# Optimization experiments

Measured on AMD Instinct MI355X. Metric: run time of the kernel, lower is better.

The kernel has to match this reference:

```python
import jax, jax.numpy as jnp
import numpy as np

ALPHA = 0.2   # LeakyReLU negative slope (init arg alpha)
H = 256       # hidden_dim
U = 1024      # user pairs -> 2U user nodes
M = 64        # UAV nodes
D = 2 * U     # uniform out-degree per UAV (edges sorted by source)
N = 2 * U + M
E = M * D


def _lstm_dir(x, w_ih, w_hh, b):
    # x: [T, B, I] -> outputs [T, B, Hc]; b = b_ih + b_hh (they only ever add)
    Hc = w_hh.shape[1]
    B = x.shape[1]
    def step(carry, xt):
        h, c = carry
        g = xt @ w_ih.T + h @ w_hh.T + b          # [B, 4*Hc], gate order i,f,g,o
        i, f, gg, o = jnp.split(g, 4, axis=-1)
        c = jax.nn.sigmoid(f) * c + jax.nn.sigmoid(i) * jnp.tanh(gg)
        h = jax.nn.sigmoid(o) * jnp.tanh(c)
        return (h, c), h
    h0 = jnp.zeros((B, Hc), x.dtype)
    _, hs = jax.lax.scan(step, (h0, h0), x)
    return hs


def _bilstm(x, wih, whh, b):
    # wih: [2, 4Hc, I]; whh: [2, 4Hc, Hc]; b: [2, 4Hc]; dir 0 = fwd, 1 = reverse
    fwd = _lstm_dir(x, wih[0], whh[0], b[0])
    rev = _lstm_dir(x[::-1], wih[1], whh[1], b[1])[::-1]
    return jnp.concatenate([fwd, rev], axis=-1)   # [T, B, 2*Hc]


def _mlp2(h, w1, b1, w2, b2):
    h = jax.nn.relu(h @ w1.T + b1)
    return jax.nn.relu(h @ w2.T + b2)


def _forward(x, edge_index, users_num,
             ul_wih, ul_whh, ul_b, uav_lin_w, uav_lin_b,
             msg_w1, msg_b1, msg_w2, msg_b2,
             wq_w, wq_b, wr_w, wr_b, att_w, att_b,
             upd_w1, upd_b1, upd_w2, upd_b2,
             uavl_wih, uavl_whh, uavl_b, lin2_w, lin2_b):
    Un = users_num
    n = x.shape[0]
    m = n - 2 * Un
    # ---- users bidirectional LSTM over the pair (seq_len=2, batch=U) ----
    seq = jnp.stack([x[:Un], x[Un:2 * Un]], axis=0)        # [2, U, 2]
    users = _bilstm(seq, ul_wih, ul_whh, ul_b)             # [2, U, H]
    users = jnp.concatenate([users[0], users[1]], axis=0)  # [2U, H]
    uavs = x[2 * Un:] @ uav_lin_w.T + uav_lin_b            # [M, H]
    h = jnp.concatenate([users, uavs], axis=0)             # [N, H]
    # ---- message passing (flow target_to_source: i=src, aggregate at src) ----
    src, tgt = edge_index[0], edge_index[1]
    xi = h[src]                                            # [E, H]
    xj = h[tgt]                                            # [E, H]
    msg = _mlp2(jnp.concatenate([xi, xj], axis=1), msg_w1, msg_b1, msg_w2, msg_b2)  # [E, H]
    q = xi @ wq_w.T + wq_b
    r = msg @ wr_w.T + wr_b
    a = jax.nn.leaky_relu(jnp.concatenate([q, r], axis=1) @ att_w.T + att_b, ALPHA)  # [E,1]
    # segment softmax: edges sorted by source, uniform degree -> reshape [M, D]
    a = jax.nn.softmax(a.reshape(m, -1), axis=1).reshape(-1, 1)
    # ---- scatter-mean aggregate over source index ----
    agg = jax.ops.segment_sum(a * msg, src, num_segments=n)          # [N, H]
    cnt = jax.ops.segment_sum(jnp.ones((src.shape[0],), x.dtype), src, num_segments=n)
    agg = agg / jnp.maximum(cnt, 1.0)[:, None]
    # ---- update ----
    h2 = _mlp2(jnp.concatenate([agg, h], axis=1), upd_w1, upd_b1, upd_w2, upd_b2)  # [N, H]
    uav_seq = h2[2 * Un:][:, None, :]                      # [M, 1, H]
    uav_out = _bilstm(uav_seq, uavl_wih, uavl_whh, uavl_b)[:, 0, :]  # [M, H]
    out = jnp.concatenate([h2[:2 * Un], uav_out], axis=0)
    return jax.nn.sigmoid(out @ lin2_w.T + lin2_b)         # [N, 2]


def setup_inputs():
    key = jax.random.key(0)
    ks = iter(jax.random.split(key, 32))
    p = lambda *s: jax.random.normal(next(ks), s, jnp.float32) * 0.05
    Hc = H // 2
    x = jax.random.uniform(next(ks), (N, 2), jnp.float32)
    src = jnp.repeat(2 * U + jnp.arange(M), D)
    tgt = jnp.tile(jnp.arange(2 * U), M)
    edge_index = jnp.stack([src, tgt]).astype(jnp.int32)
    return dict(
        x=x, edge_index=edge_index, users_num=U,
        ul_wih=p(2, 4 * Hc, 2), ul_whh=p(2, 4 * Hc, Hc), ul_b=p(2, 4 * Hc),
        uav_lin_w=p(H, 2), uav_lin_b=p(H),
        msg_w1=p(H, 2 * H), msg_b1=p(H), msg_w2=p(H, H), msg_b2=p(H),
        wq_w=p(H, H), wq_b=p(H), wr_w=p(H, H), wr_b=p(H),
        att_w=p(1, 2 * H), att_b=p(1),
        upd_w1=p(H, 2 * H), upd_b1=p(H), upd_w2=p(H, H), upd_b2=p(H),
        uavl_wih=p(2, 4 * Hc, H), uavl_whh=p(2, 4 * Hc, Hc), uavl_b=p(2, 4 * Hc),
        lin2_w=p(2, H), lin2_b=p(2),
    )


def reference(x, edge_index, users_num,
              ul_wih, ul_whh, ul_b, uav_lin_w, uav_lin_b,
              msg_w1, msg_b1, msg_w2, msg_b2,
              wq_w, wq_b, wr_w, wr_b, att_w, att_b,
              upd_w1, upd_b1, upd_w2, upd_b2,
              uavl_wih, uavl_whh, uavl_b, lin2_w, lin2_b):
    return _forward(x, edge_index, users_num,
                    ul_wih, ul_whh, ul_b, uav_lin_w, uav_lin_b,
                    msg_w1, msg_b1, msg_w2, msg_b2,
                    wq_w, wq_b, wr_w, wr_b, att_w, att_b,
                    upd_w1, upd_b1, upd_w2, upd_b2,
                    uavl_wih, uavl_whh, uavl_b, lin2_w, lin2_b)
```

## Files before the change

### kernel.cpp

```cpp
#include <hip/hip_runtime.h>
#include <hip/hip_bf16.h>
#include <math.h>

#define UQ   1024
#define NUQ  2048
#define MQ   64
#define NN   2112
#define HD   256

typedef __attribute__((ext_vector_type(4))) float f32x4;
typedef __attribute__((ext_vector_type(2))) float f32x2;
typedef __attribute__((ext_vector_type(8))) __bf16 bf16x8;

#define OFF_HB    0u
#define OFF_HUF   65536u
#define OFF_PUBF  1146880u
#define OFF_PB    2195456u
#define OFF_SPR   2260992u
#define OFF_ATT   2261248u
#define OFF_WHHT  2263552u
#define OFF_WIHT  2787840u
#define OFF_W1F   3836416u
#define OFF_W2F   4098560u
#define OFF_UW1F  4229632u
#define OFF_UW2F  4491776u
#define OFF_CREC  4622848u
#define OFF_H2U   5155328u
#define OFF_PART  5220864u

__device__ __forceinline__ float sigm(float v) { return 1.f / (1.f + expf(-v)); }

__device__ __forceinline__ int huf_idx(int row, int k) {
  return (((row >> 6) * 8 + (k >> 5)) * 4 + ((row >> 4) & 3)) * 512 +
         (((k >> 3) & 3) * 16 + (row & 15)) * 8 + (k & 7);
}

__device__ __forceinline__ void gl16(const void* g, void* l) {
  __builtin_amdgcn_global_load_lds((const __attribute__((address_space(1))) void*)g,
                                   (__attribute__((address_space(3))) void*)l, 16, 0, 0);
}

__device__ __forceinline__ int2 pack_fp8x8(const float v[8]) {
  int lo = 0, hi = 0;
  lo = __builtin_amdgcn_cvt_pk_fp8_f32(v[0], v[1], lo, false);
  lo = __builtin_amdgcn_cvt_pk_fp8_f32(v[2], v[3], lo, true);
  hi = __builtin_amdgcn_cvt_pk_fp8_f32(v[4], v[5], hi, false);
  hi = __builtin_amdgcn_cvt_pk_fp8_f32(v[6], v[7], hi, true);
  return make_int2(lo, hi);
}

__device__ void tile_transpose_perm(const float* __restrict__ in, int in_ld,
                                    float* __restrict__ out, int out_ld,
                                    int k0, int c0) {
  __shared__ float ldt[64][68];
  const int t = threadIdx.x;
  {
    const int ci = t >> 2, kq = t & 3;
    const int c = c0 + ci;
    const int row = (c & 3) * 128 + (c >> 2);
    const float* src = in + row * in_ld + k0 + kq * 16;
#pragma unroll
    for (int e = 0; e < 4; ++e)
      *(f32x4*)&ldt[ci][kq * 16 + e * 4] = *(const f32x4*)(src + e * 4);
  }
  __syncthreads();
  {
    const int kk = t >> 2, cq = t & 3;
    float* dst = out + (k0 + kk) * out_ld + c0 + cq * 16;
#pragma unroll
    for (int e4 = 0; e4 < 4; ++e4) {
      f32x4 v;
#pragma unroll
      for (int j = 0; j < 4; ++j) v[j] = ldt[cq * 16 + e4 * 4 + j][kk];
      *(f32x4*)(dst + e4 * 4) = v;
    }
  }
}

template<int K>
__device__ void frag_cast16(const float* __restrict__ W, int j0, __bf16* __restrict__ frag) {
  __shared__ float ldc[16][K + 4];
  const int t = threadIdx.x;
  {
    const int jr = t >> 4, kq = t & 15;
    const float* src = W + (j0 + jr) * K + kq * (K / 16);
#pragma unroll
    for (int e = 0; e < K / 64; ++e)
      *(f32x4*)&ldc[jr][kq * (K / 16) + e * 4] = *(const f32x4*)(src + e * 4);
  }
  __syncthreads();
  const int f = j0 >> 4;
  constexpr int nks = K >> 5;
  constexpr int thr_per_ks = 256 / nks;
  constexpr int q_per_thr = 512 / thr_per_ks;
  const int ks = t / thr_per_ks;
  const int q0 = (t % thr_per_ks) * q_per_thr;
#pragma unroll
  for (int h = 0; h < q_per_thr / 8; ++h) {
    bf16x8 v;
#pragma unroll
    for (int e = 0; e < 8; ++e) {
      int q = q0 + h * 8 + e;
      int lane = q >> 3;
      v[e] = (__bf16)ldc[lane & 15][ks * 32 + (lane >> 4) * 8 + (q & 7)];
    }
    *(bf16x8*)(frag + (ks * 16 + f) * 512 + q0 + h * 8) = v;
  }
}

__device__ void frag_cast16_fp8(const float* __restrict__ W, int j0, char* __restrict__ frag) {
  __shared__ float ldc[16][260];
  const int t = threadIdx.x;
  {
    const int jr = t >> 4, kq = t & 15;
    const float* src = W + (j0 + jr) * 256 + kq * 16;
#pragma unroll
    for (int e = 0; e < 4; ++e)
      *(f32x4*)&ldc[jr][kq * 16 + e * 4] = *(const f32x4*)(src + e * 4);
  }
  __syncthreads();
  const int f = j0 >> 4;
  const int ks = t >> 5;
  const int q0 = (t & 31) * 16;
#pragma unroll
  for (int h = 0; h < 2; ++h) {
    const int qb = q0 + h * 8;
    const int lane = qb >> 3;
    float v[8];
#pragma unroll
    for (int e = 0; e < 8; ++e)
      v[e] = ldc[lane & 15][ks * 32 + (lane >> 4) * 8 + e];
    *(int2*)(frag + (ks * 16 + f) * 512 + qb) = pack_fp8x8(v);
  }
}

__global__ __launch_bounds__(256) void k0_prep(
    const float* __restrict__ ul_whh, const float* __restrict__ uavl_wih,
    const float* __restrict__ msg_w1, const float* __restrict__ msg_w2,
    const float* __restrict__ upd_w1, const float* __restrict__ upd_w2,
    const float* __restrict__ att_w,  const float* __restrict__ att_b,
    const float* __restrict__ wq_w,   const float* __restrict__ wq_b,
    const float* __restrict__ wr_w,   const float* __restrict__ wr_b,
    char* __restrict__ ws)
{
  const int b = blockIdx.x, t = threadIdx.x;
  if (b < 32) {
    const int dir = b >> 4, tile = b & 15;
    tile_transpose_perm(ul_whh + dir * 65536, 128,
                        (float*)(ws + OFF_WHHT) + dir * 65536, 512,
                        (tile >> 3) * 64, (tile & 7) * 64);
  } else if (b < 96) {
    const int b2 = b - 32, dir = b2 >> 5, tile = b2 & 31;
    tile_transpose_perm(uavl_wih + dir * 131072, 256,
                        (float*)(ws + OFF_WIHT) + dir * 131072, 512,
                        (tile >> 3) * 64, (tile & 7) * 64);
  } else if (b < 112) {
    frag_cast16_fp8(msg_w2, (b - 96) * 16, (char*)(ws + OFF_W2F));
  } else if (b < 128) {
    frag_cast16<512>(msg_w1, (b - 112) * 16, (__bf16*)(ws + OFF_W1F));
  } else if (b < 144) {
    frag_cast16<512>(upd_w1, (b - 128) * 16, (__bf16*)(ws + OFF_UW1F));
  } else if (b < 160) {
    frag_cast16<256>(upd_w2, (b - 144) * 16, (__bf16*)(ws + OFF_UW2F));
  } else {
    float* wqa = (float*)(ws + OFF_ATT);
    float* vv  = wqa + 256;
    float* c0  = wqa + 512;
    float sa = 0.f, sr = 0.f;
    for (int j = 0; j < 256; ++j) {
      sa += att_w[j]       * wq_w[j * 256 + t];
      sr += att_w[256 + j] * wr_w[j * 256 + t];
    }
    wqa[t] = sa; vv[t] = sr;
    __shared__ float red[256];
    red[t] = att_w[t] * wq_b[t] + att_w[256 + t] * wr_b[t];
    __syncthreads();
    for (int s = 128; s > 0; s >>= 1) { if (t < s) red[t] += red[t + s]; __syncthreads(); }
    if (t == 0) c0[0] = red[0] + att_b[0];
  }
}

__global__ __launch_bounds__(256) void k1_embed(
    const float* __restrict__ x, const float* __restrict__ ul_wih,
    const float* __restrict__ ul_b, const float* __restrict__ uav_lin_w,
    const float* __restrict__ uav_lin_b, char* __restrict__ ws)
{
  __bf16* huf = (__bf16*)(ws + OFF_HUF);
  const int b = blockIdx.x, tid = threadIdx.x;
  if (b < 256) {
    const float* whhT = (const float*)(ws + OFF_WHHT);
    const int dir = tid >> 7, hc = tid & 127;
    const int u0 = b * 4;
    float wx[4], wy[4], bb[4];
#pragma unroll
    for (int g = 0; g < 4; ++g) {
      int row = g * 128 + hc;
      wx[g] = ul_wih[dir * 1024 + row * 2 + 0];
      wy[g] = ul_wih[dir * 1024 + row * 2 + 1];
      bb[g] = ul_b[dir * 512 + row];
    }
    __shared__ float h1s[2][128][4];
    __shared__ float hout[8][260];
    float c1[4], h1v[4], in1x[4], in1y[4];
#pragma unroll
    for (int uu = 0; uu < 4; ++uu) {
      int u = u0 + uu;
      float ax = x[u * 2], ay = x[u * 2 + 1];
      float bx = x[(UQ + u) * 2], by = x[(UQ + u) * 2 + 1];
      float i0x = dir ? bx : ax, i0y = dir ? by : ay;
      in1x[uu] = dir ? ax : bx; in1y[uu] = dir ? ay : by;
      float gv[4];
#pragma unroll
      for (int g = 0; g < 4; ++g) gv[g] = wx[g] * i0x + wy[g] * i0y + bb[g];
      float ii = sigm(gv[0]), gg = tanhf(gv[2]), oo = sigm(gv[3]);
      c1[uu] = ii * gg;
      h1v[uu] = oo * tanhf(c1[uu]);
      h1s[dir][hc][uu] = h1v[uu];
    }
    __syncthreads();
    float acc[4][4];
#pragma unroll
    for (int uu = 0; uu < 4; ++uu)
#pragma unroll
      for (int g = 0; g < 4; ++g) acc[uu][g] = wx[g] * in1x[uu] + wy[g] * in1y[uu] + bb[g];
#pragma unroll 4
    for (int k = 0; k < 128; ++k) {
      f32x4 hv  = *(const f32x4*)&h1s[dir][k][0];
      f32x4 wv4 = *(const f32x4*)(whhT + dir * 65536 + k * 512 + hc * 4);
#pragma unroll
      for (int uu = 0; uu < 4; ++uu)
#pragma unroll
        for (int g = 0; g < 4; ++g) acc[uu][g] += hv[uu] * wv4[g];
    }
    const int col = dir * 128 + hc;
#pragma unroll
    for (int uu = 0; uu < 4; ++uu) {
      float ii = sigm(acc[uu][0]), ff = sigm(acc[uu][1]);
      float gg = tanhf(acc[uu][2]), oo = sigm(acc[uu][3]);
      float c2 = ff * c1[uu] + ii * gg;
      float h2v = oo * tanhf(c2);
      float va = dir ? h2v : h1v[uu];
      float vb = dir ? h1v[uu] : h2v;
      hout[uu][col] = va;
      hout[4 + uu][col] = vb;
    }
    __syncthreads();
    {
      const int lr = tid >> 5, c = tid & 31;
      bf16x8 v;
#pragma unroll
      for (int e = 0; e < 8; ++e) v[e] = (__bf16)hout[lr][c * 8 + e];
      const int node = (lr < 4) ? (u0 + lr) : (UQ + u0 + lr - 4);
      *(bf16x8*)(huf + huf_idx(node, c * 8)) = v;
    }
  } else {
    float* hb = (float*)(ws + OFF_HB);
    const int j = tid;
    const int mb = (b - 256) * 16;
    for (int m = mb; m < mb + 16; ++m) {
      float xa = x[(NUQ + m) * 2], xb = x[(NUQ + m) * 2 + 1];
      float val = xa * uav_lin_w[j * 2] + xb * uav_lin_w[j * 2 + 1] + uav_lin_b[j];
      hb[m * 256 + j] = val;
      huf[huf_idx(NUQ + m, j)] = (__bf16)val;
    }
  }
}

template<int G, int NKS>
__device__ __forceinline__ void frag_gemm_acc_g(const __bf16* __restrict__ Abase, int g0,
                                                const __bf16* __restrict__ Bbase,
                                                f32x4 acc[G][4]) {
  const int lane = threadIdx.x & 63;
  const int cg = (threadIdx.x >> 6) & 3;
  for (int ks = 0; ks < NKS; ++ks) {
    bf16x8 Af[G], Bf[4];
#pragma unroll
    for (int g = 0; g < G; ++g)
      Af[g] = *(const bf16x8*)(Abase + ((ks * 4 + g0 + g) * 64 + lane) * 8);
#pragma unroll
    for (int f = 0; f < 4; ++f)
      Bf[f] = *(const bf16x8*)(Bbase + ((ks * 16 + cg * 4 + f) * 64 + lane) * 8);
#pragma unroll
    for (int g = 0; g < G; ++g)
#pragma unroll
      for (int f = 0; f < 4; ++f)
        acc[g][f] = __builtin_amdgcn_mfma_f32_16x16x32_bf16(Af[g], Bf[f], acc[g][f], 0, 0, 0);
  }
}

__global__ __launch_bounds__(256) void k2_proj(const float* __restrict__ msg_b1,
                                               char* __restrict__ ws)
{
  const __bf16* huf = (const __bf16*)(ws + OFF_HUF);
  const __bf16* w1f = (const __bf16*)(ws + OFF_W1F);
  const int b = blockIdx.x;
  const int tid = threadIdx.x;
  const int lane = tid & 63, cg = tid >> 6;
  const int cl = lane & 15, g16 = lane >> 4;
  if (b < 64) {
    f32x4 acc[2][4] = {};
    frag_gemm_acc_g<2, 8>(huf + (b >> 1) * 16384, (b & 1) * 2, w1f + 65536, acc);
    __shared__ float ldt[32][264];
#pragma unroll
    for (int g = 0; g < 2; ++g)
#pragma unroll
      for (int f = 0; f < 4; ++f)
#pragma unroll
        for (int r = 0; r < 4; ++r)
          ldt[g * 16 + g16 * 4 + r][cg * 64 + f * 16 + cl] = acc[g][f][r];
    __syncthreads();
    char* pubf = (char*)(ws + OFF_PUBF);
    const int c2 = b >> 3, r16base = (b & 7) * 2;
#pragma unroll
    for (int p = 0; p < 4; ++p) {
      const int region = p * 4 + (tid >> 6);
      const int ks = region >> 1, r16l = region & 1;
      const int row15 = tid & 15, kg = (tid >> 4) & 3;
      const int row = r16l * 16 + row15;
      float v[8];
#pragma unroll
      for (int j = 0; j < 8; ++j) v[j] = ldt[row][ks * 32 + kg * 8 + j];
      const int dst = ((c2 * 8 + ks) * 16 + (r16base + r16l)) * 512 + (kg * 16 + row15) * 8;
      *(int2*)(pubf + dst) = pack_fp8x8(v);
    }
  } else if (b == 64) {
    f32x4 acc[4][4] = {};
    frag_gemm_acc_g<4, 8>(huf + 32 * 16384, 0, w1f, acc);
    float* pb = (float*)(ws + OFF_PB);
#pragma unroll
    for (int g = 0; g < 4; ++g)
#pragma unroll
      for (int f = 0; f < 4; ++f)
#pragma unroll
        for (int r = 0; r < 4; ++r) {
          int row = g * 16 + g16 * 4 + r;
          int col = cg * 64 + f * 16 + cl;
          pb[row * 256 + col] = acc[g][f][r] + msg_b1[col];
        }
  } else {
    const float* hb  = (const float*)(ws + OFF_HB);
    const float* wqa = (const float*)(ws + OFF_ATT);
    const float* c0  = wqa + 512;
    float* spr = (float*)(ws + OFF_SPR);
    if (tid < 64) {
      float s = 0.f;
      for (int k = 0; k < 256; ++k) s += hb[tid * 256 + k] * wqa[k];
      spr[tid] = s + c0[0];
    }
  }
}

__global__ __launch_bounds__(1024, 2) void k3_edge(const float* __restrict__ msg_b2,
                                                   char* __restrict__ ws)
{
  const char*  PUBF = (const char*)(ws + OFF_PUBF);
  const float* PB   = (const float*)(ws + OFF_PB);
  const float* spr  = (const float*)(ws + OFF_SPR);
  const float* vv   = (const float*)(ws + OFF_ATT) + 256;
  const char*  W2F  = (const char*)(ws + OFF_W2F);
  float* crec = (float*)(ws + OFF_CREC);

  __shared__ __align__(16) char bufA[2][8192];
  __shared__ __align__(16) char bufB[2][8192];
  __shared__ float plds[16][64];
  __shared__ float redmax[16], wds[16];
  __shared__ float wvs[4][256];

  const int m = blockIdx.x >> 3, ch = blockIdx.x & 7;
  const int tid = threadIdx.x, wave = tid >> 6, lane = tid & 63;
  const int cl = lane & 15, g16 = lane >> 4;
  const int rg = wave >> 2, cg = wave & 3;
  const int rot = (m + ch) & 7;
  const float sm = spr[m];
  const char* Asrc = PUBF + ch * 65536;
  const float* pbm = PB + m * 256;
  const int bq = ((tid >> 4) & 3) * 8;

  auto repack = [](int2 raw, f32x4 p0, f32x4 p1) -> int2 {
    f32x2 a01 = __builtin_amdgcn_cvt_pk_f32_fp8(raw.x, false);
    f32x2 a23 = __builtin_amdgcn_cvt_pk_f32_fp8(raw.x, true);
    f32x2 a45 = __builtin_amdgcn_cvt_pk_f32_fp8(raw.y, false);
    f32x2 a67 = __builtin_amdgcn_cvt_pk_f32_fp8(raw.y, true);
    float v[8];
    v[0] = fmaxf(a01.x + p0[0], 0.f);
    v[1] = fmaxf(a01.y + p0[1], 0.f);
    v[2] = fmaxf(a23.x + p0[2], 0.f);
    v[3] = fmaxf(a23.y + p0[3], 0.f);
    v[4] = fmaxf(a45.x + p1[0], 0.f);
    v[5] = fmaxf(a45.y + p1[1], 0.f);
    v[6] = fmaxf(a67.x + p1[2], 0.f);
    v[7] = fmaxf(a67.y + p1[3], 0.f);
    return pack_fp8x8(v);
  };

  {
    int2 raw = *(const int2*)(Asrc + rot * 8192 + tid * 8);
    if (wave < 8)
      gl16(W2F + rot * 8192 + wave * 1024 + lane * 16, &bufB[0][wave * 1024 + lane * 16]);
    const float* pbp = pbm + rot * 32 + bq;
    f32x4 p0 = *(const f32x4*)pbp, p1 = *(const f32x4*)(pbp + 4);
    *(int2*)(&bufA[0][tid * 8]) = repack(raw, p0, p1);
  }
  __syncthreads();

  f32x4 acc[4][4] = {};
  for (int i = 0; i < 8; ++i) {
    const int cur = i & 1;
    int2 arn = make_int2(0, 0);
    f32x4 pn0{}, pn1{};
    if (i < 7) {
      const int ksn = (i + 1 + rot) & 7;
      arn = *(const int2*)(Asrc + ksn * 8192 + tid * 8);
      if (wave < 8)
        gl16(W2F + ksn * 8192 + wave * 1024 + lane * 16, &bufB[cur ^ 1][wave * 1024 + lane * 16]);
      const float* pbp = pbm + ksn * 32 + bq;
      pn0 = *(const f32x4*)pbp;
      pn1 = *(const f32x4*)(pbp + 4);
    }
    long Af[4], Bf[4];
#pragma unroll
    for (int g = 0; g < 4; ++g)
      Af[g] = *(const long*)(&bufA[cur][((rg * 4 + g) * 64 + lane) * 8]);
#pragma unroll
    for (int f = 0; f < 4; ++f)
      Bf[f] = *(const long*)(&bufB[cur][((cg * 4 + f) * 64 + lane) * 8]);
    __builtin_amdgcn_s_setprio(1);
#pragma unroll
    for (int g = 0; g < 4; ++g)
#pragma unroll
      for (int f = 0; f < 4; ++f)
        acc[g][f] = __builtin_amdgcn_mfma_f32_16x16x32_fp8_fp8(Af[g], Bf[f], acc[g][f], 0, 0, 0);
    __builtin_amdgcn_s_setprio(0);
    if (i < 7) {
      *(int2*)(&bufA[cur ^ 1][tid * 8]) = repack(arn, pn0, pn1);
    }
    __syncthreads();
  }

  float p[4][4] = {};
#pragma unroll
  for (int f = 0; f < 4; ++f) {
    const int j = cg * 64 + f * 16 + cl;
    const float b2j = msg_b2[j], vj = vv[j];
#pragma unroll
    for (int g = 0; g < 4; ++g)
#pragma unroll
      for (int r = 0; r < 4; ++r) {
        float mv = fmaxf(acc[g][f][r] + b2j, 0.f);
        acc[g][f][r] = mv;
        p[g][r] += mv * vj;
      }
  }
#pragma unroll
  for (int mask = 1; mask < 16; mask <<= 1)
#pragma unroll
    for (int g = 0; g < 4; ++g)
#pragma unroll
      for (int r = 0; r < 4; ++r) p[g][r] += __shfl_xor(p[g][r], mask);
  if (cl == 0) {
#pragma unroll
    for (int g = 0; g < 4; ++g)
#pragma unroll
      for (int r = 0; r < 4; ++r) plds[wave][g * 16 + g16 * 4 + r] = p[g][r];
  }
  __syncthreads();

  float lr[4][4], wm = -3.4e38f;
#pragma unroll
  for (int g = 0; g < 4; ++g)
#pragma unroll
    for (int r = 0; r < 4; ++r) {
      int row = g * 16 + g16 * 4 + r;
      float l = plds[rg * 4 + 0][row] + plds[rg * 4 + 1][row] +
                plds[rg * 4 + 2][row] + plds[rg * 4 + 3][row] + sm;
      l = l > 0.f ? l : 0.2f * l;
      lr[g][r] = l;
      wm = fmaxf(wm, l);
    }
  wm = fmaxf(wm, __shfl_xor(wm, 16));
  wm = fmaxf(wm, __shfl_xor(wm, 32));
  if (lane == 0) redmax[wave] = wm;
  __syncthreads();
  float Mc = redmax[0];
#pragma unroll
  for (int i = 1; i < 16; ++i) Mc = fmaxf(Mc, redmax[i]);

  float e[4][4], ds = 0.f;
#pragma unroll
  for (int g = 0; g < 4; ++g)
#pragma unroll
    for (int r = 0; r < 4; ++r) { e[g][r] = __expf(lr[g][r] - Mc); ds += e[g][r]; }
  ds += __shfl_xor(ds, 16);
  ds += __shfl_xor(ds, 32);
  if (lane == 0) wds[wave] = ds;

#pragma unroll
  for (int f = 0; f < 4; ++f) {
    float w = 0.f;
#pragma unroll
    for (int g = 0; g < 4; ++g)
#pragma unroll
      for (int r = 0; r < 4; ++r) w += e[g][r] * acc[g][f][r];
    w += __shfl_xor(w, 16);
    w += __shfl_xor(w, 32);
    if (g16 == 0) wvs[rg][cg * 64 + f * 16 + cl] = w;
  }
  __syncthreads();

  float* rec = crec + (m * 8 + ch) * 260;
  if (tid < 256) rec[tid] = wvs[0][tid] + wvs[1][tid] + wvs[2][tid] + wvs[3][tid];
  if (tid == 0) rec[256] = Mc;
  if (tid == 1) rec[257] = wds[0] + wds[4] + wds[8] + wds[12];
}

__global__ __launch_bounds__(256) void k56_update(
    const float* __restrict__ upd_b1, const float* __restrict__ upd_b2,
    const float* __restrict__ lin2_w, const float* __restrict__ lin2_b,
    float* __restrict__ out, char* __restrict__ ws)
{
  const __bf16* huf  = (const __bf16*)(ws + OFF_HUF);
  const __bf16* uw1f = (const __bf16*)(ws + OFF_UW1F);
  const __bf16* uw2f = (const __bf16*)(ws + OFF_UW2F);

  __shared__ __align__(16) __bf16 l1f[8 * 2 * 512];
  __shared__ __align__(16) __bf16 aggf[8 * 2 * 512];
  __shared__ float scs[32][8];
  __shared__ float sS[32];
  __shared__ float l2p[4][32][2];

  const int b = blockIdx.x, tid = threadIdx.x;
  const int lane = tid & 63, cg = tid >> 6;
  const int cl = lane & 15, g16 = lane >> 4;

  f32x4 acc[2][4] = {};
  if (b < 64) {
    frag_gemm_acc_g<2, 8>(huf + (b >> 1) * 16384, (b & 1) * 2, uw1f + 8 * 16 * 512, acc);
  } else {
    const int m0 = (b - 64) * 32;
    const float* crec = (const float*)(ws + OFF_CREC);
    if (tid < 32) {
      const int m = m0 + tid;
      float mx = -3.4e38f;
      for (int c = 0; c < 8; ++c) mx = fmaxf(mx, crec[(m * 8 + c) * 260 + 256]);
      float S = 0.f;
      for (int c = 0; c < 8; ++c) {
        float sc = __expf(crec[(m * 8 + c) * 260 + 256] - mx);
        scs[tid][c] = sc;
        S += sc * crec[(m * 8 + c) * 260 + 257];
      }
      sS[tid] = S;
    }
    __syncthreads();
    for (int ml = 0; ml < 32; ++ml) {
      float A = 0.f;
#pragma unroll
      for (int c = 0; c < 8; ++c) A += scs[ml][c] * crec[((m0 + ml) * 8 + c) * 260 + tid];
      float agg = A / sS[ml] * (1.f / 2048.f);
      aggf[((tid >> 5) * 2 + (ml >> 4)) * 512 + (((tid >> 3) & 3) * 16 + (ml & 15)) * 8 + (tid & 7)] =
          (__bf16)agg;
    }
    __syncthreads();
    const int g0 = (b - 64) * 2;
    const __bf16* hufu = huf + 32 * 16384;
    for (int ks = 0; ks < 8; ++ks) {
      bf16x8 Af[2], Bf[4];
#pragma unroll
      for (int g = 0; g < 2; ++g)
        Af[g] = *(const bf16x8*)(aggf + ((ks * 2 + g) * 64 + lane) * 8);
#pragma unroll
      for (int f = 0; f < 4; ++f)
        Bf[f] = *(const bf16x8*)(uw1f + ((ks * 16 + cg * 4 + f) * 64 + lane) * 8);
#pragma unroll
      for (int g = 0; g < 2; ++g)
#pragma unroll
        for (int f = 0; f < 4; ++f)
          acc[g][f] = __builtin_amdgcn_mfma_f32_16x16x32_bf16(Af[g], Bf[f], acc[g][f], 0, 0, 0);
    }
    for (int ks = 8; ks < 16; ++ks) {
      bf16x8 Af[2], Bf[4];
#pragma unroll
      for (int g = 0; g < 2; ++g)
        Af[g] = *(const bf16x8*)(hufu + (((ks - 8) * 4 + g0 + g) * 64 + lane) * 8);
#pragma unroll
      for (int f = 0; f < 4; ++f)
        Bf[f] = *(const bf16x8*)(uw1f + ((ks * 16 + cg * 4 + f) * 64 + lane) * 8);
#pragma unroll
      for (int g = 0; g < 2; ++g)
#pragma unroll
        for (int f = 0; f < 4; ++f)
          acc[g][f] = __builtin_amdgcn_mfma_f32_16x16x32_bf16(Af[g], Bf[f], acc[g][f], 0, 0, 0);
    }
  }

#pragma unroll
  for (int g = 0; g < 2; ++g)
#pragma unroll
    for (int f = 0; f < 4; ++f) {
      const int col = cg * 64 + f * 16 + cl;
      const float b1 = upd_b1[col];
#pragma unroll
      for (int r = 0; r < 4; ++r) {
        float v = fmaxf(acc[g][f][r] + b1, 0.f);
        l1f[((col >> 5) * 2 + g) * 512 + (((col >> 3) & 3) * 16 + g16 * 4 + r) * 8 + (col & 7)] =
            (__bf16)v;
      }
    }
  __syncthreads();

  f32x4 a2[2][4] = {};
  for (int ks = 0; ks < 8; ++ks) {
    bf16x8 Af[2], Bf[4];
#pragma unroll
    for (int g = 0; g < 2; ++g)
      Af[g] = *(const bf16x8*)(l1f + ((ks * 2 + g) * 64 + lane) * 8);
#pragma unroll
    for (int f = 0; f < 4; ++f)
      Bf[f] = *(const bf16x8*)(uw2f + ((ks * 16 + cg * 4 + f) * 64 + lane) * 8);
#pragma unroll
    for (int g = 0; g < 2; ++g)
#pragma unroll
      for (int f = 0; f < 4; ++f)
        a2[g][f] = __builtin_amdgcn_mfma_f32_16x16x32_bf16(Af[g], Bf[f], a2[g][f], 0, 0, 0);
  }

  if (b < 64) {
    float d0[2][4] = {}, d1[2][4] = {};
#pragma unroll
    for (int f = 0; f < 4; ++f) {
      const int col = cg * 64 + f * 16 + cl;
      const float b2 = upd_b2[col];
      const float w0 = lin2_w[col], w1 = lin2_w[256 + col];
#pragma unroll
      for (int g = 0; g < 2; ++g)
#pragma unroll
        for (int r = 0; r < 4; ++r) {
          float hv = fmaxf(a2[g][f][r] + b2, 0.f);
          d0[g][r] += hv * w0;
          d1[g][r] += hv * w1;
        }
    }
#pragma unroll
    for (int mask = 1; mask < 16; mask <<= 1)
#pragma unroll
      for (int g = 0; g < 2; ++g)
#pragma unroll
        for (int r = 0; r < 4; ++r) {
          d0[g][r] += __shfl_xor(d0[g][r], mask);
          d1[g][r] += __shfl_xor(d1[g][r], mask);
        }
    if (cl == 0) {
#pragma unroll
      for (int g = 0; g < 2; ++g)
#pragma unroll
        for (int r = 0; r < 4; ++r) {
          l2p[cg][g * 16 + g16 * 4 + r][0] = d0[g][r];
          l2p[cg][g * 16 + g16 * 4 + r][1] = d1[g][r];
        }
    }
    __syncthreads();
    if (tid < 32) {
      float s0 = l2p[0][tid][0] + l2p[1][tid][0] + l2p[2][tid][0] + l2p[3][tid][0] + lin2_b[0];
      float s1 = l2p[0][tid][1] + l2p[1][tid][1] + l2p[2][tid][1] + l2p[3][tid][1] + lin2_b[1];
      const int row = b * 32 + tid;
      out[row * 2 + 0] = 1.f / (1.f + expf(-s0));
      out[row * 2 + 1] = 1.f / (1.f + expf(-s1));
    }
  } else {
    float* h2u = (float*)(ws + OFF_H2U);
    const int m0 = (b - 64) * 32;
#pragma unroll
    for (int g = 0; g < 2; ++g)
#pragma unroll
      for (int f = 0; f < 4; ++f) {
        const int col = cg * 64 + f * 16 + cl;
        const float b2 = upd_b2[col];
#pragma unroll
        for (int r = 0; r < 4; ++r) {
          const int rl = g * 16 + g16 * 4 + r;
          h2u[(m0 + rl) * 256 + col] = fmaxf(a2[g][f][r] + b2, 0.f);
        }
      }
  }
}

__global__ __launch_bounds__(256) void k7a_gates(char* __restrict__ ws)
{
  const float* h2u  = (const float*)(ws + OFF_H2U);
  const float* wihT = (const float*)(ws + OFF_WIHT);
  float* part = (float*)(ws + OFF_PART);
  const int m = blockIdx.x >> 2, kq = blockIdx.x & 3;
  const int tid = threadIdx.x;
  const int dir = tid >> 7, hc = tid & 127;
  __shared__ float xs[64];
  if (tid < 64) xs[tid] = h2u[m * 256 + kq * 64 + tid];
  __syncthreads();
  f32x4 a4 = {0.f, 0.f, 0.f, 0.f};
  for (int k = 0; k < 64; ++k) {
    float xv = xs[k];
    f32x4 wv4 = *(const f32x4*)(wihT + dir * 131072 + (kq * 64 + k) * 512 + hc * 4);
#pragma unroll
    for (int g = 0; g < 4; ++g) a4[g] += xv * wv4[g];
  }
  *(f32x4*)(part + (m * 4 + kq) * 1024 + dir * 512 + hc * 4) = a4;
}

__global__ __launch_bounds__(256) void k7b_final(
    const float* __restrict__ uavl_b, const float* __restrict__ lin2_w,
    const float* __restrict__ lin2_b, float* __restrict__ out, char* __restrict__ ws)
{
  const float* part = (const float*)(ws + OFF_PART);
  const int m = blockIdx.x, tid = threadIdx.x;
  const int dir = tid >> 7, hc = tid & 127;
  f32x4 a4 = {0.f, 0.f, 0.f, 0.f};
#pragma unroll
  for (int kq = 0; kq < 4; ++kq) {
    f32x4 p = *(const f32x4*)(part + (m * 4 + kq) * 1024 + dir * 512 + hc * 4);
#pragma unroll
    for (int g = 0; g < 4; ++g) a4[g] += p[g];
  }
  float bb[4];
#pragma unroll
  for (int g = 0; g < 4; ++g) bb[g] = uavl_b[dir * 512 + g * 128 + hc];
  __shared__ float uo[256];
  float ii = sigm(a4[0] + bb[0]);
  float gg = tanhf(a4[2] + bb[2]);
  float oo = sigm(a4[3] + bb[3]);
  float cc = ii * gg;
  uo[dir * 128 + hc] = oo * tanhf(cc);
  __syncthreads();
  float p0 = uo[tid] * lin2_w[tid];
  float p1 = uo[tid] * lin2_w[256 + tid];
#pragma unroll
  for (int mask = 1; mask < 64; mask <<= 1) {
    p0 += __shfl_xor(p0, mask);
    p1 += __shfl_xor(p1, mask);
  }
  __shared__ float r0s[4], r1s[4];
  const int lane = tid & 63, wv = tid >> 6;
  if (lane == 0) { r0s[wv] = p0; r1s[wv] = p1; }
  __syncthreads();
  if (tid == 0) {
    float d0 = r0s[0] + r0s[1] + r0s[2] + r0s[3] + lin2_b[0];
    float d1 = r1s[0] + r1s[1] + r1s[2] + r1s[3] + lin2_b[1];
    out[(NUQ + m) * 2 + 0] = 1.f / (1.f + expf(-d0));
    out[(NUQ + m) * 2 + 1] = 1.f / (1.f + expf(-d1));
  }
}

extern "C" void kernel_launch(void* const* d_in, const int* in_sizes, int n_in,
                              void* d_out, int out_size, void* d_ws, size_t ws_size,
                              hipStream_t stream)
{
  const float* x         = (const float*)d_in[0];
  const float* ul_wih    = (const float*)d_in[3];
  const float* ul_whh    = (const float*)d_in[4];
  const float* ul_b      = (const float*)d_in[5];
  const float* uav_lin_w = (const float*)d_in[6];
  const float* uav_lin_b = (const float*)d_in[7];
  const float* msg_w1    = (const float*)d_in[8];
  const float* msg_b1    = (const float*)d_in[9];
  const float* msg_w2    = (const float*)d_in[10];
  const float* msg_b2    = (const float*)d_in[11];
  const float* wq_w      = (const float*)d_in[12];
  const float* wq_b      = (const float*)d_in[13];
  const float* wr_w      = (const float*)d_in[14];
  const float* wr_b      = (const float*)d_in[15];
  const float* att_w     = (const float*)d_in[16];
  const float* att_b     = (const float*)d_in[17];
  const float* upd_w1    = (const float*)d_in[18];
  const float* upd_b1    = (const float*)d_in[19];
  const float* upd_w2    = (const float*)d_in[20];
  const float* upd_b2    = (const float*)d_in[21];
  const float* uavl_wih  = (const float*)d_in[22];
  const float* uavl_b    = (const float*)d_in[24];
  const float* lin2_w    = (const float*)d_in[25];
  const float* lin2_b    = (const float*)d_in[26];
  char* ws = (char*)d_ws;
  float* out = (float*)d_out;

  k0_prep<<<dim3(161), dim3(256), 0, stream>>>(ul_whh, uavl_wih, msg_w1, msg_w2, upd_w1,
                                               upd_w2, att_w, att_b, wq_w, wq_b, wr_w, wr_b, ws);
  k1_embed<<<dim3(260), dim3(256), 0, stream>>>(x, ul_wih, ul_b, uav_lin_w, uav_lin_b, ws);
  k2_proj<<<dim3(66), dim3(256), 0, stream>>>(msg_b1, ws);
  k3_edge<<<dim3(512), dim3(1024), 0, stream>>>(msg_b2, ws);
  k56_update<<<dim3(66), dim3(256), 0, stream>>>(upd_b1, upd_b2, lin2_w, lin2_b, out, ws);
  k7a_gates<<<dim3(256), dim3(256), 0, stream>>>(ws);
  k7b_final<<<dim3(64), dim3(256), 0, stream>>>(uavl_b, lin2_w, lin2_b, out, ws);
}
```

Measured before the change: 92.54 us.

## Fuse update, UAV LSTM gates and final linear into one kernel with fp16 MFMA

```diff
diff --git a/kernel.cpp b/kernel.cpp
--- a/kernel.cpp
+++ b/kernel.cpp
@@ -1,5 +1,6 @@
 #include <hip/hip_runtime.h>
 #include <hip/hip_bf16.h>
+#include <hip/hip_fp16.h>
 #include <math.h>
 
 #define UQ   1024
@@ -11,22 +12,22 @@
 typedef __attribute__((ext_vector_type(4))) float f32x4;
 typedef __attribute__((ext_vector_type(2))) float f32x2;
 typedef __attribute__((ext_vector_type(8))) __bf16 bf16x8;
+typedef __attribute__((ext_vector_type(8))) _Float16 f16x8;
 
 #define OFF_HB    0u
 #define OFF_HUF   65536u
 #define OFF_PUBF  1146880u
-#define OFF_PB    2195456u
-#define OFF_SPR   2260992u
-#define OFF_ATT   2261248u
-#define OFF_WHHT  2263552u
-#define OFF_WIHT  2787840u
-#define OFF_W1F   3836416u
-#define OFF_W2F   4098560u
-#define OFF_UW1F  4229632u
-#define OFF_UW2F  4491776u
-#define OFF_CREC  4622848u
-#define OFF_H2U   5155328u
-#define OFF_PART  5220864u
+#define OFF_PB    1671168u
+#define OFF_SPR   1736704u
+#define OFF_ATT   1736960u
+#define OFF_WHHT  1739264u
+#define OFF_W1F   2263552u
+#define OFF_W2F   2525696u
+#define OFF_UW1F  2591232u
+#define OFF_UW2F  2853376u
+#define OFF_CREC  2984448u
+#define OFF_WIHF  3516928u
+#define OFF_H2UF  4041216u
 
 __device__ __forceinline__ float sigm(float v) { return 1.f / (1.f + expf(-v)); }
 
@@ -149,19 +150,38 @@
     tile_transpose_perm(ul_whh + dir * 65536, 128,
                         (float*)(ws + OFF_WHHT) + dir * 65536, 512,
                         (tile >> 3) * 64, (tile & 7) * 64);
+  } else if (b < 48) {
+    frag_cast16_fp8(msg_w2, (b - 32) * 16, (char*)(ws + OFF_W2F));
+  } else if (b < 64) {
+    frag_cast16<512>(msg_w1, (b - 48) * 16, (__bf16*)(ws + OFF_W1F));
+  } else if (b < 80) {
+    frag_cast16<512>(upd_w1, (b - 64) * 16, (__bf16*)(ws + OFF_UW1F));
   } else if (b < 96) {
-    const int b2 = b - 32, dir = b2 >> 5, tile = b2 & 31;
-    tile_transpose_perm(uavl_wih + dir * 131072, 256,
-                        (float*)(ws + OFF_WIHT) + dir * 131072, 512,
-                        (tile >> 3) * 64, (tile & 7) * 64);
-  } else if (b < 112) {
-    frag_cast16_fp8(msg_w2, (b - 96) * 16, (char*)(ws + OFF_W2F));
-  } else if (b < 128) {
-    frag_cast16<512>(msg_w1, (b - 112) * 16, (__bf16*)(ws + OFF_W1F));
-  } else if (b < 144) {
-    frag_cast16<512>(upd_w1, (b - 128) * 16, (__bf16*)(ws + OFF_UW1F));
+    frag_cast16<256>(upd_w2, (b - 80) * 16, (__bf16*)(ws + OFF_UW2F));
   } else if (b < 160) {
-    frag_cast16<256>(upd_w2, (b - 144) * 16, (__bf16*)(ws + OFF_UW2F));
+    __shared__ float ldc2[16][260];
+    const int b2 = b - 96;
+    {
+      const int jr = t >> 4, kq = t & 15;
+      const int jp = b2 * 16 + jr;
+      const int dir = jp >> 9, rem = jp & 511, hc = rem >> 2, gg = rem & 3;
+      const float* src = uavl_wih + (dir * 512 + gg * 128 + hc) * 256 + kq * 16;
+#pragma unroll
+      for (int e = 0; e < 4; ++e)
+        *(f32x4*)&ldc2[jr][kq * 16 + e * 4] = *(const f32x4*)(src + e * 4);
+    }
+    __syncthreads();
+    _Float16* wf = (_Float16*)(ws + OFF_WIHF);
+    const int ks = t >> 5, sub = t & 31;
+#pragma unroll
+    for (int i = 0; i < 2; ++i) {
+      const int gp = sub * 2 + i;
+      const int cl = gp & 15, g16 = gp >> 4;
+      _Float16 v[8];
+#pragma unroll
+      for (int e = 0; e < 8; ++e) v[e] = (_Float16)ldc2[cl][ks * 32 + g16 * 8 + e];
+      *(ulong2*)(wf + (ks * 64 + b2) * 512 + (g16 * 16 + cl) * 8) = *(ulong2*)v;
+    }
   } else {
     float* wqa = (float*)(ws + OFF_ATT);
     float* vv  = wqa + 256;
@@ -513,117 +533,56 @@
   if (tid == 1) rec[257] = wds[0] + wds[4] + wds[8] + wds[12];
 }
 
-__global__ __launch_bounds__(256) void k56_update(
+__global__ __launch_bounds__(1024) void k567_update(
     const float* __restrict__ upd_b1, const float* __restrict__ upd_b2,
-    const float* __restrict__ lin2_w, const float* __restrict__ lin2_b,
-    float* __restrict__ out, char* __restrict__ ws)
+    const float* __restrict__ uavl_b, const float* __restrict__ lin2_w,
+    const float* __restrict__ lin2_b, float* __restrict__ out, char* __restrict__ ws)
 {
+  __shared__ __align__(16) char smem[135168];
   const __bf16* huf  = (const __bf16*)(ws + OFF_HUF);
   const __bf16* uw1f = (const __bf16*)(ws + OFF_UW1F);
   const __bf16* uw2f = (const __bf16*)(ws + OFF_UW2F);
-
-  __shared__ __align__(16) __bf16 l1f[8 * 2 * 512];
-  __shared__ __align__(16) __bf16 aggf[8 * 2 * 512];
-  __shared__ float scs[32][8];
-  __shared__ float sS[32];
-  __shared__ float l2p[4][32][2];
-
   const int b = blockIdx.x, tid = threadIdx.x;
-  const int lane = tid & 63, cg = tid >> 6;
+  const int lane = tid & 63, cg = (tid >> 6) & 3;
   const int cl = lane & 15, g16 = lane >> 4;
-
-  f32x4 acc[2][4] = {};
-  if (b < 64) {
-    frag_gemm_acc_g<2, 8>(huf + (b >> 1) * 16384, (b & 1) * 2, uw1f + 8 * 16 * 512, acc);
-  } else {
-    const int m0 = (b - 64) * 32;
-    const float* crec = (const float*)(ws + OFF_CREC);
-    if (tid < 32) {
-      const int m = m0 + tid;
-      float mx = -3.4e38f;
-      for (int c = 0; c < 8; ++c) mx = fmaxf(mx, crec[(m * 8 + c) * 260 + 256]);
-      float S = 0.f;
-      for (int c = 0; c < 8; ++c) {
-        float sc = __expf(crec[(m * 8 + c) * 260 + 256] - mx);
-        scs[tid][c] = sc;
-        S += sc * crec[(m * 8 + c) * 260 + 257];
+  const int q = tid >> 8;
+
+  if (b < 16) {
+    __bf16* l1f = (__bf16*)smem + q * 8192;
+    float*  l2p = (float*)(smem + 65536);
+    f32x4 acc[2][4] = {};
+    frag_gemm_acc_g<2, 8>(huf + (b * 2 + (q >> 1)) * 16384, (q & 1) * 2,
+                          uw1f + 8 * 16 * 512, acc);
+#pragma unroll
+    for (int g = 0; g < 2; ++g)
+#pragma unroll
+      for (int f = 0; f < 4; ++f) {
+        const int col = cg * 64 + f * 16 + cl;
+        const float b1 = upd_b1[col];
+#pragma unroll
+        for (int r = 0; r < 4; ++r) {
+          float v = fmaxf(acc[g][f][r] + b1, 0.f);
+          l1f[((col >> 5) * 2 + g) * 512 + (((col >> 3) & 3) * 16 + g16 * 4 + r) * 8 + (col & 7)] =
+              (__bf16)v;
+        }
       }
-      sS[tid] = S;
-    }
-    __syncthreads();
-    for (int ml = 0; ml < 32; ++ml) {
-      float A = 0.f;
-#pragma unroll
-      for (int c = 0; c < 8; ++c) A += scs[ml][c] * crec[((m0 + ml) * 8 + c) * 260 + tid];
-      float agg = A / sS[ml] * (1.f / 2048.f);
-      aggf[((tid >> 5) * 2 + (ml >> 4)) * 512 + (((tid >> 3) & 3) * 16 + (ml & 15)) * 8 + (tid & 7)] =
-          (__bf16)agg;
-    }
-    __syncthreads();
-    const int g0 = (b - 64) * 2;
-    const __bf16* hufu = huf + 32 * 16384;
+    __syncthreads();
+
+    f32x4 a2[2][4] = {};
     for (int ks = 0; ks < 8; ++ks) {
       bf16x8 Af[2], Bf[4];
 #pragma unroll
       for (int g = 0; g < 2; ++g)
-        Af[g] = *(const bf16x8*)(aggf + ((ks * 2 + g) * 64 + lane) * 8);
+        Af[g] = *(const bf16x8*)(l1f + ((ks * 2 + g) * 64 + lane) * 8);
 #pragma unroll
       for (int f = 0; f < 4; ++f)
-        Bf[f] = *(const bf16x8*)(uw1f + ((ks * 16 + cg * 4 + f) * 64 + lane) * 8);
+        Bf[f] = *(const bf16x8*)(uw2f + ((ks * 16 + cg * 4 + f) * 64 + lane) * 8);
 #pragma unroll
       for (int g = 0; g < 2; ++g)
 #pragma unroll
         for (int f = 0; f < 4; ++f)
-          acc[g][f] = __builtin_amdgcn_mfma_f32_16x16x32_bf16(Af[g], Bf[f], acc[g][f], 0, 0, 0);
-    }
-    for (int ks = 8; ks < 16; ++ks) {
-      bf16x8 Af[2], Bf[4];
-#pragma unroll
-      for (int g = 0; g < 2; ++g)
-        Af[g] = *(const bf16x8*)(hufu + (((ks - 8) * 4 + g0 + g) * 64 + lane) * 8);
-#pragma unroll
-      for (int f = 0; f < 4; ++f)
-        Bf[f] = *(const bf16x8*)(uw1f + ((ks * 16 + cg * 4 + f) * 64 + lane) * 8);
-#pragma unroll
-      for (int g = 0; g < 2; ++g)
-#pragma unroll
-        for (int f = 0; f < 4; ++f)
-          acc[g][f] = __builtin_amdgcn_mfma_f32_16x16x32_bf16(Af[g], Bf[f], acc[g][f], 0, 0, 0);
-    }
-  }
-
-#pragma unroll
-  for (int g = 0; g < 2; ++g)
-#pragma unroll
-    for (int f = 0; f < 4; ++f) {
-      const int col = cg * 64 + f * 16 + cl;
-      const float b1 = upd_b1[col];
-#pragma unroll
-      for (int r = 0; r < 4; ++r) {
-        float v = fmaxf(acc[g][f][r] + b1, 0.f);
-        l1f[((col >> 5) * 2 + g) * 512 + (((col >> 3) & 3) * 16 + g16 * 4 + r) * 8 + (col & 7)] =
-            (__bf16)v;
-      }
-    }
-  __syncthreads();
-
-  f32x4 a2[2][4] = {};
-  for (int ks = 0; ks < 8; ++ks) {
-    bf16x8 Af[2], Bf[4];
-#pragma unroll
-    for (int g = 0; g < 2; ++g)
-      Af[g] = *(const bf16x8*)(l1f + ((ks * 2 + g) * 64 + lane) * 8);
-#pragma unroll
-    for (int f = 0; f < 4; ++f)
-      Bf[f] = *(const bf16x8*)(uw2f + ((ks * 16 + cg * 4 + f) * 64 + lane) * 8);
-#pragma unroll
-    for (int g = 0; g < 2; ++g)
-#pragma unroll
-      for (int f = 0; f < 4; ++f)
-        a2[g][f] = __builtin_amdgcn_mfma_f32_16x16x32_bf16(Af[g], Bf[f], a2[g][f], 0, 0, 0);
-  }
-
-  if (b < 64) {
+          a2[g][f] = __builtin_amdgcn_mfma_f32_16x16x32_bf16(Af[g], Bf[f], a2[g][f], 0, 0, 0);
+    }
     float d0[2][4] = {}, d1[2][4] = {};
 #pragma unroll
     for (int f = 0; f < 4; ++f) {
@@ -653,97 +612,176 @@
       for (int g = 0; g < 2; ++g)
 #pragma unroll
         for (int r = 0; r < 4; ++r) {
-          l2p[cg][g * 16 + g16 * 4 + r][0] = d0[g][r];
-          l2p[cg][g * 16 + g16 * 4 + r][1] = d1[g][r];
+          const int r32 = g * 16 + g16 * 4 + r;
+          l2p[((q * 4 + cg) * 32 + r32) * 2 + 0] = d0[g][r];
+          l2p[((q * 4 + cg) * 32 + r32) * 2 + 1] = d1[g][r];
         }
     }
     __syncthreads();
-    if (tid < 32) {
-      float s0 = l2p[0][tid][0] + l2p[1][tid][0] + l2p[2][tid][0] + l2p[3][tid][0] + lin2_b[0];
-      float s1 = l2p[0][tid][1] + l2p[1][tid][1] + l2p[2][tid][1] + l2p[3][tid][1] + lin2_b[1];
-      const int row = b * 32 + tid;
+    if (tid < 128) {
+      const int qq = tid >> 5, r32 = tid & 31;
+      float s0 = lin2_b[0], s1 = lin2_b[1];
+#pragma unroll
+      for (int c = 0; c < 4; ++c) {
+        s0 += l2p[((qq * 4 + c) * 32 + r32) * 2 + 0];
+        s1 += l2p[((qq * 4 + c) * 32 + r32) * 2 + 1];
+      }
+      const int row = b * 128 + qq * 32 + r32;
       out[row * 2 + 0] = 1.f / (1.f + expf(-s0));
       out[row * 2 + 1] = 1.f / (1.f + expf(-s1));
     }
-  } else {
-    float* h2u = (float*)(ws + OFF_H2U);
-    const int m0 = (b - 64) * 32;
-#pragma unroll
-    for (int g = 0; g < 2; ++g)
+    return;
+  }
+
+  const float* crec = (const float*)(ws + OFF_CREC);
+  __bf16* aggf = (__bf16*)smem;
+  __bf16* l1fu = (__bf16*)(smem + 32768);
+  float* ldt = (float*)smem;
+  float* uo  = (float*)(smem + 66816);
+  float* scs = (float*)(smem + 132352);
+  float* sS  = (float*)(smem + 134400);
+  _Float16* h2uf = (_Float16*)(ws + OFF_H2UF);
+  const _Float16* wihf = (const _Float16*)(ws + OFF_WIHF);
+
+  if (tid < 64) {
+    const int m = tid;
+    float mx = -3.4e38f;
+    for (int c = 0; c < 8; ++c) mx = fmaxf(mx, crec[(m * 8 + c) * 260 + 256]);
+    float S = 0.f;
+    for (int c = 0; c < 8; ++c) {
+      float sc = __expf(crec[(m * 8 + c) * 260 + 256] - mx);
+      scs[m * 8 + c] = sc;
+      S += sc * crec[(m * 8 + c) * 260 + 257];
+    }
+    sS[m] = S;
+  }
+  __syncthreads();
+  {
+    const int k = tid & 255, m4 = tid >> 8;
+#pragma unroll
+    for (int i = 0; i < 16; ++i) {
+      const int ml = m4 + i * 4;
+      float A = 0.f;
+#pragma unroll
+      for (int c = 0; c < 8; ++c) A += scs[ml * 8 + c] * crec[(ml * 8 + c) * 260 + k];
+      float agg = A / sS[ml] * (1.f / 2048.f);
+      aggf[((k >> 5) * 4 + (ml >> 4)) * 512 + (((k >> 3) & 3) * 16 + (ml & 15)) * 8 + (k & 7)] =
+          (__bf16)agg;
+    }
+  }
+  __syncthreads();
+
+  const __bf16* hufu = huf + 32 * 16384;
+  f32x4 acc1[4] = {};
+  for (int ks = 0; ks < 8; ++ks) {
+    bf16x8 Af = *(const bf16x8*)(aggf + ((ks * 4 + q) * 64 + lane) * 8);
+#pragma unroll
+    for (int f = 0; f < 4; ++f) {
+      bf16x8 Bf = *(const bf16x8*)(uw1f + ((ks * 16 + cg * 4 + f) * 64 + lane) * 8);
+      acc1[f] = __builtin_amdgcn_mfma_f32_16x16x32_bf16(Af, Bf, acc1[f], 0, 0, 0);
+    }
+  }
+  for (int ks = 8; ks < 16; ++ks) {
+    bf16x8 Af = *(const bf16x8*)(hufu + (((ks - 8) * 4 + q) * 64 + lane) * 8);
+#pragma unroll
+    for (int f = 0; f < 4; ++f) {
+      bf16x8 Bf = *(const bf16x8*)(uw1f + ((ks * 16 + cg * 4 + f) * 64 + lane) * 8);
+      acc1[f] = __builtin_amdgcn_mfma_f32_16x16x32_bf16(Af, Bf, acc1[f], 0, 0, 0);
+    }
+  }
+#pragma unroll
+  for (int f = 0; f < 4; ++f) {
+    const int col = cg * 64 + f * 16 + cl;
+    const float b1 = upd_b1[col];
+#pragma unroll
+    for (int r = 0; r < 4; ++r) {
+      float v = fmaxf(acc1[f][r] + b1, 0.f);
+      l1fu[((col >> 5) * 4 + q) * 512 + (((col >> 3) & 3) * 16 + g16 * 4 + r) * 8 + (col & 7)] =
+          (__bf16)v;
+    }
+  }
+  __syncthreads();
+
+  f32x4 acc2[4] = {};
+  for (int ks = 0; ks < 8; ++ks) {
+    bf16x8 Af = *(const bf16x8*)(l1fu + ((ks * 4 + q) * 64 + lane) * 8);
+#pragma unroll
+    for (int f = 0; f < 4; ++f) {
+      bf16x8 Bf = *(const bf16x8*)(uw2f + ((ks * 16 + cg * 4 + f) * 64 + lane) * 8);
+      acc2[f] = __builtin_amdgcn_mfma_f32_16x16x32_bf16(Af, Bf, acc2[f], 0, 0, 0);
+    }
+  }
+#pragma unroll
+  for (int f = 0; f < 4; ++f) {
+    const int col = cg * 64 + f * 16 + cl;
+    const float b2 = upd_b2[col];
+#pragma unroll
+    for (int r = 0; r < 4; ++r) {
+      const int rl = g16 * 4 + r;
+      float v = fmaxf(acc2[f][r] + b2, 0.f);
+      h2uf[((col >> 5) * 4 + q) * 512 + (((col >> 3) & 3) * 16 + rl) * 8 + (col & 7)] =
+          (_Float16)v;
+    }
+  }
+  __syncthreads();
+
+  const int w = tid >> 6;
+  const int rgq = w >> 2, cf = w & 3;
+  for (int q2 = 0; q2 < 4; ++q2) {
+    f32x4 ga[4] = {};
+    for (int ks = 0; ks < 8; ++ks) {
+      f16x8 Af = *(const f16x8*)(h2uf + ((ks * 4 + rgq) * 64 + lane) * 8);
 #pragma unroll
       for (int f = 0; f < 4; ++f) {
-        const int col = cg * 64 + f * 16 + cl;
-        const float b2 = upd_b2[col];
-#pragma unroll
-        for (int r = 0; r < 4; ++r) {
-          const int rl = g * 16 + g16 * 4 + r;
-          h2u[(m0 + rl) * 256 + col] = fmaxf(a2[g][f][r] + b2, 0.f);
-        }
+        f16x8 Bf = *(const f16x8*)(wihf + ((ks * 64 + q2 * 16 + cf * 4 + f) * 64 + lane) * 8);
+        ga[f] = __builtin_amdgcn_mfma_f32_16x16x32_f16(Af, Bf, ga[f], 0, 0, 0);
       }
-  }
-}
-
-__global__ __launch_bounds__(256) void k7a_gates(char* __restrict__ ws)
-{
-  const float* h2u  = (const float*)(ws + OFF_H2U);
-  const float* wihT = (const float*)(ws + OFF_WIHT);
-  float* part = (float*)(ws + OFF_PART);
-  const int m = blockIdx.x >> 2, kq = blockIdx.x & 3;
-  const int tid = threadIdx.x;
-  const int dir = tid >> 7, hc = tid & 127;
-  __shared__ float xs[64];
-  if (tid < 64) xs[tid] = h2u[m * 256 + kq * 64 + tid];
-  __syncthreads();
-  f32x4 a4 = {0.f, 0.f, 0.f, 0.f};
-  for (int k = 0; k < 64; ++k) {
-    float xv = xs[k];
-    f32x4 wv4 = *(const f32x4*)(wihT + dir * 131072 + (kq * 64 + k) * 512 + hc * 4);
-#pragma unroll
-    for (int g = 0; g < 4; ++g) a4[g] += xv * wv4[g];
-  }
-  *(f32x4*)(part + (m * 4 + kq) * 1024 + dir * 512 + hc * 4) = a4;
-}
-
-__global__ __launch_bounds__(256) void k7b_final(
-    const float* __restrict__ uavl_b, const float* __restrict__ lin2_w,
-    const float* __restrict__ lin2_b, float* __restrict__ out, char* __restrict__ ws)
-{
-  const float* part = (const float*)(ws + OFF_PART);
-  const int m = blockIdx.x, tid = threadIdx.x;
-  const int dir = tid >> 7, hc = tid & 127;
-  f32x4 a4 = {0.f, 0.f, 0.f, 0.f};
-#pragma unroll
-  for (int kq = 0; kq < 4; ++kq) {
-    f32x4 p = *(const f32x4*)(part + (m * 4 + kq) * 1024 + dir * 512 + hc * 4);
-#pragma unroll
-    for (int g = 0; g < 4; ++g) a4[g] += p[g];
-  }
-  float bb[4];
-#pragma unroll
-  for (int g = 0; g < 4; ++g) bb[g] = uavl_b[dir * 512 + g * 128 + hc];
-  __shared__ float uo[256];
-  float ii = sigm(a4[0] + bb[0]);
-  float gg = tanhf(a4[2] + bb[2]);
-  float oo = sigm(a4[3] + bb[3]);
-  float cc = ii * gg;
-  uo[dir * 128 + hc] = oo * tanhf(cc);
-  __syncthreads();
-  float p0 = uo[tid] * lin2_w[tid];
-  float p1 = uo[tid] * lin2_w[256 + tid];
-#pragma unroll
-  for (int mask = 1; mask < 64; mask <<= 1) {
-    p0 += __shfl_xor(p0, mask);
-    p1 += __shfl_xor(p1, mask);
-  }
-  __shared__ float r0s[4], r1s[4];
-  const int lane = tid & 63, wv = tid >> 6;
-  if (lane == 0) { r0s[wv] = p0; r1s[wv] = p1; }
-  __syncthreads();
-  if (tid == 0) {
-    float d0 = r0s[0] + r0s[1] + r0s[2] + r0s[3] + lin2_b[0];
-    float d1 = r1s[0] + r1s[1] + r1s[2] + r1s[3] + lin2_b[1];
-    out[(NUQ + m) * 2 + 0] = 1.f / (1.f + expf(-d0));
-    out[(NUQ + m) * 2 + 1] = 1.f / (1.f + expf(-d1));
+    }
+#pragma unroll
+    for (int f = 0; f < 4; ++f) {
+      const int collocal = cf * 64 + f * 16 + cl;
+      const int jp = q2 * 256 + collocal;
+      const int dir = jp >> 9, rem = jp & 511, hc = rem >> 2, gt = rem & 3;
+      const float bias = uavl_b[dir * 512 + gt * 128 + hc];
+#pragma unroll
+      for (int r = 0; r < 4; ++r)
+        ldt[(rgq * 16 + g16 * 4 + r) * 260 + collocal] = ga[f][r] + bias;
+    }
+    __syncthreads();
+    {
+      const int dir = q2 >> 1, hcb = (q2 & 1) * 64;
+#pragma unroll
+      for (int i = 0; i < 4; ++i) {
+        const int idx = i * 1024 + tid;
+        const int m = idx & 63, hcl = idx >> 6;
+        float ii = sigm(ldt[m * 260 + hcl * 4 + 0]);
+        float gg = tanhf(ldt[m * 260 + hcl * 4 + 2]);
+        float oo = sigm(ldt[m * 260 + hcl * 4 + 3]);
+        uo[m * 256 + dir * 128 + hcb + hcl] = oo * tanhf(ii * gg);
+      }
+    }
+    __syncthreads();
+  }
+
+  {
+    const int m = tid >> 4, c16 = tid & 15;
+    float p0 = 0.f, p1 = 0.f;
+#pragma unroll
+    for (int e = 0; e < 16; ++e) {
+      const int c = c16 * 16 + e;
+      float u = uo[m * 256 + c];
+      p0 += u * lin2_w[c];
+      p1 += u * lin2_w[256 + c];
+    }
+#pragma unroll
+    for (int mask = 1; mask < 16; mask <<= 1) {
+      p0 += __shfl_xor(p0, mask);
+      p1 += __shfl_xor(p1, mask);
+    }
+    if (c16 == 0) {
+      out[(NUQ + m) * 2 + 0] = 1.f / (1.f + expf(-(p0 + lin2_b[0])));
+      out[(NUQ + m) * 2 + 1] = 1.f / (1.f + expf(-(p1 + lin2_b[1])));
+    }
   }
 }
 
@@ -783,7 +821,6 @@
   k1_embed<<<dim3(260), dim3(256), 0, stream>>>(x, ul_wih, ul_b, uav_lin_w, uav_lin_b, ws);
   k2_proj<<<dim3(66), dim3(256), 0, stream>>>(msg_b1, ws);
   k3_edge<<<dim3(512), dim3(1024), 0, stream>>>(msg_b2, ws);
-  k56_update<<<dim3(66), dim3(256), 0, stream>>>(upd_b1, upd_b2, lin2_w, lin2_b, out, ws);
-  k7a_gates<<<dim3(256), dim3(256), 0, stream>>>(ws);
-  k7b_final<<<dim3(64), dim3(256), 0, stream>>>(uavl_b, lin2_w, lin2_b, out, ws);
-}
+  k567_update<<<dim3(17), dim3(1024), 0, stream>>>(upd_b1, upd_b2, uavl_b, lin2_w, lin2_b,
+                                                   out, ws);
+}
```

After: 135.7 us. +46.7%, slower.
